# Kernel tuning notes

Measured on AMD Instinct MI355X. Metric: run time of the kernel, lower is better.

## Reference

```python
import jax, jax.numpy as jnp
import numpy as np

N = 100_000        # nodes
E = 1_600_000      # edges
IN_F = 128         # input_features
HID = 64           # hiddens per head
OUT = 64           # outputs
NHEADS = 8
ALPHA = 0.2        # leaky_relu negative slope


def setup_inputs() -> dict:
    key = jax.random.key(0)
    ks = jax.random.split(key, 8)
    x = jax.random.normal(ks[0], (N, IN_F), jnp.float32)
    edges = jax.random.randint(ks[1], (2, E), 0, N)
    # nn.Linear(input_features, input_features)
    W0 = jax.random.normal(ks[2], (IN_F, IN_F), jnp.float32) / np.sqrt(IN_F).astype(np.float32)
    b0 = jnp.zeros((IN_F,), jnp.float32)
    # per-head SpGAT params: W [in, out], a [2*out]
    W_heads = jax.random.normal(ks[3], (NHEADS, IN_F, HID), jnp.float32) * 0.05
    a_heads = jax.random.normal(ks[4], (NHEADS, 2 * HID), jnp.float32) * 0.05
    W_end = jax.random.normal(ks[5], (NHEADS * HID, OUT), jnp.float32) * 0.05
    a_end = jax.random.normal(ks[6], (2 * OUT,), jnp.float32) * 0.05
    return dict(x=x, edges=edges, W0=W0, b0=b0,
                W_heads=W_heads, a_heads=a_heads, W_end=W_end, a_end=a_end)


def _sp_gat_layer(x, src, dst, W, a, apply_elu):
    """Standard sparse GAT layer (pyGAT SpGraphAttentionLayer).

    score_e = a . [h_src || h_dst];  e = exp(-leaky_relu(score))
    out_i = (sum_{e: src=i} e * h_dst) / (sum_{e: src=i} e)
    """
    n = x.shape[0]
    h = x @ W                      # [N, F]
    F = h.shape[1]
    # a.[h_i||h_j] decomposed into per-node scores to avoid [E, 2F] gather
    s_src = h @ a[:F]              # [N]
    s_dst = h @ a[F:]              # [N]
    score = s_src[src] + s_dst[dst]            # [E]
    edge_e = jnp.exp(-jax.nn.leaky_relu(score, ALPHA))
    rowsum = jax.ops.segment_sum(edge_e, src, num_segments=n)            # [N]
    agg = jax.ops.segment_sum(edge_e[:, None] * h[dst], src, num_segments=n)  # [N, F]
    out = agg / (rowsum[:, None] + 1e-16)
    return jax.nn.elu(out) if apply_elu else out


def reference(x, edges, W0, b0, W_heads, a_heads, W_end, a_end):
    src, dst = edges[0], edges[1]
    xp = x @ W0 + b0                                           # self.layer
    # multi-head attention, concat on feature dim (loop over fixed small head count)
    heads = [_sp_gat_layer(xp, src, dst, W_heads[i], a_heads[i], apply_elu=True)
             for i in range(NHEADS)]
    h = jnp.concatenate(heads, axis=1)                         # [N, NHEADS*HID]
    out = _sp_gat_layer(h, src, dst, W_end, a_end, apply_elu=False)  # [N, OUT]
    return jax.nn.softmax(out, axis=1)
```

## Files before the change

kernel.cpp:

```cpp
#include <hip/hip_runtime.h>


using bf16x8 = __bf16 __attribute__((ext_vector_type(8)));
using f32x4  = float  __attribute__((ext_vector_type(4)));

__device__ __forceinline__ unsigned short f2bf(float f) {
    __bf16 h = (__bf16)f;
    return __builtin_bit_cast(unsigned short, h);
}
__device__ __forceinline__ float bflo(unsigned int u) {
    return __builtin_bit_cast(float, u << 16);
}
__device__ __forceinline__ float bfhi(unsigned int u) {
    return __builtin_bit_cast(float, u & 0xffff0000u);
}
__device__ __forceinline__ float bfs(unsigned short u) {
    return __builtin_bit_cast(float, (unsigned)u << 16);
}
__device__ __forceinline__ int rdlane_i(int v, int l) {
    return __builtin_amdgcn_readlane(v, l);
}
__device__ __forceinline__ float rdlane_f(float v, int l) {
    return __builtin_bit_cast(float, __builtin_amdgcn_readlane(__builtin_bit_cast(int, v), l));
}
__device__ __forceinline__ int rfl(int v) {
    return __builtin_amdgcn_readfirstlane(v);
}
__device__ __forceinline__ float exp2fast(float x) {
#if __has_builtin(__builtin_amdgcn_exp2f)
    return __builtin_amdgcn_exp2f(x);
#else
    return exp2f(x);
#endif
}

#define ALPHA_NEG 0.2f
#define LOG2E 1.44269504088896340736f
#define CHUNK 20000
#define TILE 4096
#define VPT 16

__global__ void pack_all(const float* __restrict__ W0, const float* __restrict__ Wh,
                         const float* __restrict__ We, const float* __restrict__ ah,
                         unsigned short* __restrict__ W0t, unsigned short* __restrict__ Ballt,
                         unsigned short* __restrict__ Wendt, unsigned short* __restrict__ Bscore) {
    int b = blockIdx.x, t = threadIdx.x;
    if (b < 64) {
        int idx = b * 256 + t;
        int n = idx >> 7, k = idx & 127;
        W0t[n * 128 + k] = f2bf(W0[k * 128 + n]);
    } else if (b < 320) {
        int idx = (b - 64) * 256 + t;
        int c = idx >> 7, k = idx & 127;
        int h = c >> 6, f = c & 63;
        Ballt[idx] = f2bf(Wh[(h * 128 + k) * 64 + f]);
    } else if (b < 448) {
        int idx = (b - 320) * 256 + t;
        int n = idx >> 9, k = idx & 511;
        Wendt[idx] = f2bf(We[k * 64 + n]);
    } else {
        int idx = (b - 448) * 256 + t;
        if (idx < 1024) {
            int h = idx >> 7, k = idx & 127;
            float s = 0.f, d = 0.f;
            for (int f = 0; f < 64; f++) {
                float wv = Wh[(h * 128 + k) * 64 + f];
                s += wv * ah[h * 128 + f];
                d += wv * ah[h * 128 + 64 + f];
            }
            Bscore[h * 128 + k] = f2bf(s * LOG2E);
            Bscore[(8 + h) * 128 + k] = f2bf(d * LOG2E);
        }
    }
}

__global__ void csr_hist(const int* __restrict__ src, int* __restrict__ hb, int E) {
    __shared__ int h[512];
    int t = threadIdx.x, blk = blockIdx.x;
    h[t] = 0; h[t + 256] = 0;
    __syncthreads();
    int base = blk * TILE + t;
#pragma unroll
    for (int v = 0; v < VPT; v++) {
        int e = base + v * 256;
        if (e < E) atomicAdd(&h[src[e] >> 8], 1);
    }
    __syncthreads();
    hb[blk * 512 + t] = h[t];
    hb[blk * 512 + t + 256] = h[t + 256];
}

__global__ void csr_scan(int* __restrict__ hb, int* __restrict__ bkt_base, int ablk) {
    __shared__ int s[512];
    int t = threadIdx.x;
    int run = 0;
    for (int b0 = 0; b0 < ablk; b0 += 8) {
        int vv[8];
#pragma unroll
        for (int u = 0; u < 8; u++) {
            int blk = b0 + u;
            vv[u] = (blk < ablk) ? hb[blk * 512 + t] : 0;
        }
#pragma unroll
        for (int u = 0; u < 8; u++) {
            int blk = b0 + u;
            if (blk < ablk) hb[blk * 512 + t] = run;
            run += vv[u];
        }
    }
    s[t] = run;
    __syncthreads();
    for (int off = 1; off < 512; off <<= 1) {
        int add = (t >= off) ? s[t - off] : 0;
        __syncthreads();
        s[t] += add;
        __syncthreads();
    }
    bkt_base[t] = s[t] - run;
}

__global__ void csr_scatter(const int* __restrict__ src, const int* __restrict__ dst,
                            const int* __restrict__ hb, const int* __restrict__ bkt_base,
                            int2* __restrict__ pairs, int E) {
    __shared__ int cur[512];
    int t = threadIdx.x, blk = blockIdx.x;
    cur[t]       = hb[blk * 512 + t]       + bkt_base[t];
    cur[t + 256] = hb[blk * 512 + t + 256] + bkt_base[t + 256];
    __syncthreads();
    int base = blk * TILE + t;
#pragma unroll
    for (int v = 0; v < VPT; v++) {
        int e = base + v * 256;
        if (e < E) {
            int sv = src[e], dv = dst[e];
            int pos = atomicAdd(&cur[sv >> 8], 1);
            pairs[pos] = make_int2(sv, dv);
        }
    }
}

__global__ void csr_build(const int2* __restrict__ pairs, const int* __restrict__ bkt_base,
                          int* __restrict__ row_ptr, int* __restrict__ dstp, int n) {
    __shared__ int h[256];
    __shared__ int sc[256];
    int t = threadIdx.x, b = blockIdx.x;
    int e0 = bkt_base[b], e1 = bkt_base[b + 1];
    h[t] = 0;
    __syncthreads();
    for (int e = e0 + t; e < e1; e += 256) atomicAdd(&h[pairs[e].x & 255], 1);
    __syncthreads();
    int v = h[t];
    sc[t] = v;
    __syncthreads();
    for (int off = 1; off < 256; off <<= 1) {
        int add = (t >= off) ? sc[t - off] : 0;
        __syncthreads();
        sc[t] += add;
        __syncthreads();
    }
    int excl = sc[t] - v;
    int gid = (b << 8) + t;
    if (gid <= n) row_ptr[gid] = e0 + excl;
    h[t] = excl;
    __syncthreads();
    for (int e = e0 + t; e < e1; e += 256) {
        int2 pr = pairs[e];
        int pos = atomicAdd(&h[pr.x & 255], 1);
        dstp[e0 + pos] = pr.y;
    }
}

template <int BM, int BN, int K, int WM, int WN, int MT, int NT,
          bool AF32, bool BIAS, bool OBF16, bool ELU, bool BATCHZ>
__launch_bounds__(256)
__global__ void gemm_mfma(const void* __restrict__ Ap, const unsigned short* __restrict__ Bt,
                          const float* __restrict__ bias, void* __restrict__ Cp, int M,
                          int lda, int ldc) {
    constexpr int LDK = 40;
    __shared__ unsigned short As[BM * LDK];
    __shared__ unsigned short Bs[BN * LDK];
    const int t = threadIdx.x;
    const long m0 = (long)blockIdx.x * BM;
    const long n0 = (long)blockIdx.y * BN;
    const int abase = BATCHZ ? blockIdx.z * K : 0;
    const unsigned short* Btz = BATCHZ ? Bt + (size_t)blockIdx.z * BN * K : Bt;
    const long cbase = BATCHZ ? (long)blockIdx.z * BN : 0;
    const int wave = t >> 6, lane = t & 63;
    const int wm = wave / WN, wn = wave % WN;
    const int lrow = lane & 15, lq = lane >> 4;

    f32x4 acc[MT][NT];
#pragma unroll
    for (int a = 0; a < MT; a++)
#pragma unroll
        for (int b = 0; b < NT; b++) acc[a][b] = (f32x4)0.0f;

    for (int kt = 0; kt < K / 32; kt++) {
        const int k0 = kt * 32;
        if constexpr (AF32) {
            const float* A = (const float*)Ap;
#pragma unroll
            for (int it = 0; it < BM * 8 / 256; it++) {
                int L = t + 256 * it;
                int row = L >> 3, kc = (L & 7) * 4;
                long gr = m0 + row;
                float4 v = make_float4(0.f, 0.f, 0.f, 0.f);
                if (gr < M) v = *(const float4*)&A[gr * lda + abase + k0 + kc];
                unsigned int lo = (unsigned)f2bf(v.x) | ((unsigned)f2bf(v.y) << 16);
                unsigned int hi = (unsigned)f2bf(v.z) | ((unsigned)f2bf(v.w) << 16);
                *(uint2*)&As[row * LDK + kc] = make_uint2(lo, hi);
            }
        } else {
            const unsigned short* A = (const unsigned short*)Ap;
#pragma unroll
            for (int it = 0; it < BM * 4 / 256; it++) {
                int L = t + 256 * it;
                int row = L >> 2, kc = (L & 3) * 8;
                long gr = m0 + row;
                uint4 v = make_uint4(0u, 0u, 0u, 0u);
                if (gr < M) v = *(const uint4*)&A[gr * lda + abase + k0 + kc];
                *(uint4*)&As[row * LDK + kc] = v;
            }
        }
#pragma unroll
        for (int it = 0; it < (BN * 4 + 255) / 256; it++) {
            int L = t + 256 * it;
            if (L < BN * 4) {
                int row = L >> 2, kc = (L & 3) * 8;
                *(uint4*)&Bs[row * LDK + kc] = *(const uint4*)&Btz[(n0 + row) * K + k0 + kc];
            }
        }
        __syncthreads();

        bf16x8 af[MT], bfr[NT];
#pragma unroll
        for (int mt = 0; mt < MT; mt++)
            af[mt] = *(const bf16x8*)&As[((wm * MT + mt) * 16 + lrow) * LDK + lq * 8];
#pragma unroll
        for (int nt = 0; nt < NT; nt++)
            bfr[nt] = *(const bf16x8*)&Bs[((wn * NT + nt) * 16 + lrow) * LDK + lq * 8];
#pragma unroll
        for (int mt = 0; mt < MT; mt++)
#pragma unroll
            for (int nt = 0; nt < NT; nt++)
                acc[mt][nt] = __builtin_amdgcn_mfma_f32_16x16x32_bf16(af[mt], bfr[nt],
                                                                     acc[mt][nt], 0, 0, 0);
        __syncthreads();
    }

#pragma unroll
    for (int mt = 0; mt < MT; mt++) {
        long rbase = m0 + (wm * MT + mt) * 16 + lq * 4;
#pragma unroll
        for (int nt = 0; nt < NT; nt++) {
            long col = cbase + n0 + (wn * NT + nt) * 16 + lrow;
            float bv = 0.f;
            if constexpr (BIAS) bv = bias[col];
#pragma unroll
            for (int r = 0; r < 4; r++) {
                long row = rbase + r;
                if (row < M) {
                    float v = acc[mt][nt][r] + bv;
                    if constexpr (ELU) v = v > 0.f ? v : __expf(v) - 1.0f;
                    if constexpr (OBF16)
                        ((unsigned short*)Cp)[row * ldc + col] = f2bf(v);
                    else
                        ((float*)Cp)[row * ldc + col] = v;
                }
            }
        }
    }
}

__global__ void agg_xp(const int* __restrict__ row_ptr, const int* __restrict__ dstp,
                       const float* __restrict__ s16,
                       const unsigned short* __restrict__ xp, unsigned short* __restrict__ z,
                       int n0, int n1) {
    int t = threadIdx.x, wave = t >> 6, lane = t & 63;
    int i = n0 + blockIdx.x * 4 + wave;
    if (i >= n1) return;
    int e0 = rfl(row_ptr[i]);
    int e1 = rfl(row_ptr[i + 1]);
    const int hl = lane & 7, sub8 = lane >> 3;
    const int voff = lane << 1;
    float ssv = s16[(size_t)i * 16 + hl];
    float acc[16];
#pragma unroll
    for (int c = 0; c < 16; c++) acc[c] = 0.f;
    float rsl = 0.f;

    for (int base = e0; base < e1; base += 64) {
        int m = e1 - base; if (m > 64) m = 64;
        int jl = lane < m ? lane : m - 1;
        int jreg = dstp[base + jl];

        for (int p = 0; p < m; p += 8) {
            int rel = p + sub8;
            bool ok = rel < m;
            if (!ok) rel = m - 1;
            int jw = __shfl(jreg, rel, 64);
            float sc = s16[(size_t)(unsigned)jw * 16 + 8 + hl];
            float s = ssv + sc;
            s = fmaxf(s, ALPHA_NEG * s);
            float wv = ok ? exp2fast(-s) : 0.f;
            rsl += wv;
            int nem = m - p;
            unsigned xv[8];
#pragma unroll
            for (int u = 0; u < 8; u++) {
                if (u < nem) {
                    int ju = rdlane_i(jreg, p + u);
                    xv[u] = *(const unsigned*)&xp[(size_t)(unsigned)ju * 128 + voff];
                }
            }
#pragma unroll
            for (int u = 0; u < 8; u++) {
                if (u < nem) {
                    float lo = bflo(xv[u]), hi = bfhi(xv[u]);
#pragma unroll
                    for (int h = 0; h < 8; h++) {
                        float wh = rdlane_f(wv, u * 8 + h);
                        acc[2 * h]     += wh * lo;
                        acc[2 * h + 1] += wh * hi;
                    }
                }
            }
        }
    }

    rsl += __shfl_xor(rsl, 8, 64);
    rsl += __shfl_xor(rsl, 16, 64);
    rsl += __shfl_xor(rsl, 32, 64);
    float inv = 1.0f / (rsl + 1e-16f);
    size_t zb = (size_t)(i - n0) * 1024 + voff;
#pragma unroll
    for (int h = 0; h < 8; h++) {
        float ih = rdlane_f(inv, h);
        unsigned pw = (unsigned)f2bf(acc[2 * h] * ih) |
                      ((unsigned)f2bf(acc[2 * h + 1] * ih) << 16);
        *(unsigned*)&z[zb + h * 128] = pw;
    }
}

__global__ void scores2(const unsigned short* __restrict__ h2b, const float* __restrict__ ae,
                        float* __restrict__ ss2, float* __restrict__ sd2, int n) {
    int t = threadIdx.x, wave = t >> 6, lane = t & 63;
    int i = blockIdx.x * 4 + wave;
    if (i >= n) return;
    float v = bfs(h2b[(size_t)i * 64 + lane]);
    float a = v * ae[lane];
    float b = v * ae[64 + lane];
    for (int d = 32; d > 0; d >>= 1) {
        a += __shfl_xor(a, d, 64);
        b += __shfl_xor(b, d, 64);
    }
    if (lane == 0) { ss2[i] = a * LOG2E; sd2[i] = b * LOG2E; }
}

__global__ void agg_final(const int* __restrict__ row_ptr, const int* __restrict__ dstp,
                          const float* __restrict__ ss2, const float* __restrict__ sd2,
                          const unsigned short* __restrict__ h2b, float* __restrict__ out,
                          int n) {
    int t = threadIdx.x, wave = t >> 6, lane = t & 63;
    int i = blockIdx.x * 4 + wave;
    if (i >= n) return;
    int e0 = rfl(row_ptr[i]);
    int e1 = rfl(row_ptr[i + 1]);
    float ssrc = ss2[i];
    float acc = 0.f, rsl = 0.f;
    for (int base = e0; base < e1; base += 64) {
        int cnt = e1 - base; if (cnt > 64) cnt = 64;
        int jv = 0; float wv = 0.f;
        if (lane < cnt) {
            jv = dstp[base + lane];
            float sc = ssrc + sd2[jv];
            sc = fmaxf(sc, ALPHA_NEG * sc);
            wv = exp2fast(-sc);
        }
        rsl += wv;
        int q = 0;
        for (; q + 8 <= cnt; q += 8) {
            float vv[8], ww[8];
#pragma unroll
            for (int u = 0; u < 8; u++) {
                int j = rdlane_i(jv, q + u);
                vv[u] = bfs(h2b[((size_t)(unsigned)j << 6) + lane]);
                ww[u] = rdlane_f(wv, q + u);
            }
#pragma unroll
            for (int u = 0; u < 8; u++) acc += ww[u] * vv[u];
        }
        for (; q < cnt; q++) {
            int j = rdlane_i(jv, q);
            float w = rdlane_f(wv, q);
            acc += w * bfs(h2b[((size_t)(unsigned)j << 6) + lane]);
        }
    }
    float rs = rsl;
    for (int d = 32; d > 0; d >>= 1) rs += __shfl_xor(rs, d, 64);
    float o = acc / (rs + 1e-16f);
    float m = o;
    for (int d = 32; d > 0; d >>= 1) m = fmaxf(m, __shfl_xor(m, d, 64));
    float e = __expf(o - m);
    float s = e;
    for (int d = 32; d > 0; d >>= 1) s += __shfl_xor(s, d, 64);
    out[(size_t)i * 64 + lane] = e / s;
}

extern "C" void kernel_launch(void* const* d_in, const int* in_sizes, int n_in,
                              void* d_out, int out_size, void* d_ws, size_t ws_size,
                              hipStream_t stream) {
    const float* x  = (const float*)d_in[0];
    const int* edges = (const int*)d_in[1];
    const float* W0 = (const float*)d_in[2];
    const float* b0 = (const float*)d_in[3];
    const float* Wh = (const float*)d_in[4];
    const float* ah = (const float*)d_in[5];
    const float* We = (const float*)d_in[6];
    const float* ae = (const float*)d_in[7];
    float* dout = (float*)d_out;

    const int Nn = in_sizes[0] / 128;
    const int E  = in_sizes[1] / 2;
    const int* src = edges;
    const int* dst = edges + E;

    char* p = (char*)d_ws;
    auto alloc = [&](size_t bytes) -> char* {
        char* r = p;
        p += (bytes + 255) & ~(size_t)255;
        return r;
    };
    unsigned short* W0t   = (unsigned short*)alloc(128 * 128 * 2);
    unsigned short* Ballt = (unsigned short*)alloc(512 * 128 * 2);
    unsigned short* Wendt = (unsigned short*)alloc((size_t)64 * 512 * 2);
    unsigned short* Bscore = (unsigned short*)alloc(16 * 128 * 2);
    const int ablk = (E + TILE - 1) / TILE;
    int* hist_blk = (int*)alloc((size_t)ablk * 512 * 4);
    int* bkt_base = (int*)alloc(512 * 4);
    int* row_ptr = (int*)alloc((size_t)(Nn + 1) * 4);
    int* dstp    = (int*)alloc((size_t)E * 4);
    float* s16   = (float*)alloc((size_t)Nn * 16 * 4);
    float* ss2   = (float*)alloc((size_t)Nn * 4);
    float* sd2   = (float*)alloc((size_t)Nn * 4);
    unsigned short* xp = (unsigned short*)alloc((size_t)Nn * 128 * 2);
    unsigned short* z  = (unsigned short*)alloc((size_t)CHUNK * 1024 * 2);
    unsigned short* hcat = (unsigned short*)alloc((size_t)Nn * 512 * 2);
    unsigned short* h2b = (unsigned short*)z;
    int2* pairs = (int2*)hcat;

    size_t needed = (size_t)(p - (char*)d_ws);
    if (needed > ws_size) return;

    const int gm = (Nn + 127) / 128;
    const int nbkt = (Nn + 255) >> 8;

    pack_all<<<452, 256, 0, stream>>>(W0, Wh, We, ah, W0t, Ballt, Wendt, Bscore);

    csr_hist<<<ablk, 256, 0, stream>>>(src, hist_blk, E);
    csr_scan<<<1, 512, 0, stream>>>(hist_blk, bkt_base, ablk);
    csr_scatter<<<ablk, 256, 0, stream>>>(src, dst, hist_blk, bkt_base, pairs, E);
    csr_build<<<nbkt, 256, 0, stream>>>(pairs, bkt_base, row_ptr, dstp, Nn);

    gemm_mfma<128, 128, 128, 2, 2, 4, 4, true, true, true, false, false>
        <<<dim3(gm, 1), 256, 0, stream>>>(x, W0t, b0, xp, Nn, 128, 128);

    gemm_mfma<128, 16, 128, 4, 1, 2, 1, false, false, false, false, false>
        <<<dim3(gm, 1), 256, 0, stream>>>(xp, Bscore, nullptr, s16, Nn, 128, 16);

    for (int c0 = 0; c0 < Nn; c0 += CHUNK) {
        int c1 = min(c0 + CHUNK, Nn);
        int Mc = c1 - c0;
        agg_xp<<<(Mc + 3) / 4, 256, 0, stream>>>(row_ptr, dstp, s16, xp, z, c0, c1);
        gemm_mfma<128, 64, 128, 4, 1, 2, 4, false, false, true, true, true>
            <<<dim3((Mc + 127) / 128, 1, 8), 256, 0, stream>>>(
                z, Ballt, nullptr, hcat + (size_t)c0 * 512, Mc, 1024, 512);
    }

    gemm_mfma<128, 64, 512, 4, 1, 2, 4, false, false, true, false, false>
        <<<dim3(gm, 1), 256, 0, stream>>>(hcat, Wendt, nullptr, h2b, Nn, 512, 64);

    scores2<<<(Nn + 3) / 4, 256, 0, stream>>>(h2b, ae, ss2, sd2, Nn);
    agg_final<<<(Nn + 3) / 4, 256, 0, stream>>>(row_ptr, dstp, ss2, sd2, h2b, dout, Nn);
}
```

Baseline: 561.4 us.

## Fuse neighbor aggregation with per-head projection GEMM via shared-memory staging

Replaces the chunked agg_xp plus batched per-head GEMM launches with a single agg_gemm kernel. Each block aggregates 16 nodes into an LDS tile and immediately runs MFMA against the per-head weights, applying ELU and writing hcat directly. This removes the global round trip of the large intermediate z buffer and about ten kernel launches. In exchange, each block uses about 33 KB of LDS, which may lower occupancy for the latency-bound gather, and the B fragments are read directly from global memory.

```diff
diff --git a/kernel.cpp b/kernel.cpp
--- a/kernel.cpp
+++ b/kernel.cpp
@@ -36,9 +36,10 @@
 
 #define ALPHA_NEG 0.2f
 #define LOG2E 1.44269504088896340736f
-#define CHUNK 20000
 #define TILE 4096
 #define VPT 16
+#define NB 16
+#define LDKZ 1032
 
 __global__ void pack_all(const float* __restrict__ W0, const float* __restrict__ Wh,
                          const float* __restrict__ We, const float* __restrict__ ah,
@@ -171,7 +172,7 @@
 }
 
 template <int BM, int BN, int K, int WM, int WN, int MT, int NT,
-          bool AF32, bool BIAS, bool OBF16, bool ELU, bool BATCHZ>
+          bool AF32, bool BIAS, bool OBF16, bool ELU>
 __launch_bounds__(256)
 __global__ void gemm_mfma(const void* __restrict__ Ap, const unsigned short* __restrict__ Bt,
                           const float* __restrict__ bias, void* __restrict__ Cp, int M,
@@ -181,10 +182,6 @@
     __shared__ unsigned short Bs[BN * LDK];
     const int t = threadIdx.x;
     const long m0 = (long)blockIdx.x * BM;
-    const long n0 = (long)blockIdx.y * BN;
-    const int abase = BATCHZ ? blockIdx.z * K : 0;
-    const unsigned short* Btz = BATCHZ ? Bt + (size_t)blockIdx.z * BN * K : Bt;
-    const long cbase = BATCHZ ? (long)blockIdx.z * BN : 0;
     const int wave = t >> 6, lane = t & 63;
     const int wm = wave / WN, wn = wave % WN;
     const int lrow = lane & 15, lq = lane >> 4;
@@ -205,7 +202,7 @@
                 int row = L >> 3, kc = (L & 7) * 4;
                 long gr = m0 + row;
                 float4 v = make_float4(0.f, 0.f, 0.f, 0.f);
-                if (gr < M) v = *(const float4*)&A[gr * lda + abase + k0 + kc];
+                if (gr < M) v = *(const float4*)&A[gr * lda + k0 + kc];
                 unsigned int lo = (unsigned)f2bf(v.x) | ((unsigned)f2bf(v.y) << 16);
                 unsigned int hi = (unsigned)f2bf(v.z) | ((unsigned)f2bf(v.w) << 16);
                 *(uint2*)&As[row * LDK + kc] = make_uint2(lo, hi);
@@ -218,7 +215,7 @@
                 int row = L >> 2, kc = (L & 3) * 8;
                 long gr = m0 + row;
                 uint4 v = make_uint4(0u, 0u, 0u, 0u);
-                if (gr < M) v = *(const uint4*)&A[gr * lda + abase + k0 + kc];
+                if (gr < M) v = *(const uint4*)&A[gr * lda + k0 + kc];
                 *(uint4*)&As[row * LDK + kc] = v;
             }
         }
@@ -227,7 +224,7 @@
             int L = t + 256 * it;
             if (L < BN * 4) {
                 int row = L >> 2, kc = (L & 3) * 8;
-                *(uint4*)&Bs[row * LDK + kc] = *(const uint4*)&Btz[(n0 + row) * K + k0 + kc];
+                *(uint4*)&Bs[row * LDK + kc] = *(const uint4*)&Bt[(size_t)row * K + k0 + kc];
             }
         }
         __syncthreads();
@@ -253,7 +250,7 @@
         long rbase = m0 + (wm * MT + mt) * 16 + lq * 4;
 #pragma unroll
         for (int nt = 0; nt < NT; nt++) {
-            long col = cbase + n0 + (wn * NT + nt) * 16 + lrow;
+            long col = (wn * NT + nt) * 16 + lrow;
             float bv = 0.f;
             if constexpr (BIAS) bv = bias[col];
 #pragma unroll
@@ -272,73 +269,119 @@
     }
 }
 
-__global__ void agg_xp(const int* __restrict__ row_ptr, const int* __restrict__ dstp,
-                       const float* __restrict__ s16,
-                       const unsigned short* __restrict__ xp, unsigned short* __restrict__ z,
-                       int n0, int n1) {
+__launch_bounds__(256)
+__global__ void agg_gemm(const int* __restrict__ row_ptr, const int* __restrict__ dstp,
+                         const float* __restrict__ s16, const unsigned short* __restrict__ xp,
+                         const unsigned short* __restrict__ Ballt,
+                         unsigned short* __restrict__ hcat, int n) {
+    __shared__ unsigned short zs[NB * LDKZ];
     int t = threadIdx.x, wave = t >> 6, lane = t & 63;
-    int i = n0 + blockIdx.x * 4 + wave;
-    if (i >= n1) return;
-    int e0 = rfl(row_ptr[i]);
-    int e1 = rfl(row_ptr[i + 1]);
     const int hl = lane & 7, sub8 = lane >> 3;
     const int voff = lane << 1;
-    float ssv = s16[(size_t)i * 16 + hl];
-    float acc[16];
-#pragma unroll
-    for (int c = 0; c < 16; c++) acc[c] = 0.f;
-    float rsl = 0.f;
-
-    for (int base = e0; base < e1; base += 64) {
-        int m = e1 - base; if (m > 64) m = 64;
-        int jl = lane < m ? lane : m - 1;
-        int jreg = dstp[base + jl];
-
-        for (int p = 0; p < m; p += 8) {
-            int rel = p + sub8;
-            bool ok = rel < m;
-            if (!ok) rel = m - 1;
-            int jw = __shfl(jreg, rel, 64);
-            float sc = s16[(size_t)(unsigned)jw * 16 + 8 + hl];
-            float s = ssv + sc;
-            s = fmaxf(s, ALPHA_NEG * s);
-            float wv = ok ? exp2fast(-s) : 0.f;
-            rsl += wv;
-            int nem = m - p;
-            unsigned xv[8];
-#pragma unroll
-            for (int u = 0; u < 8; u++) {
-                if (u < nem) {
-                    int ju = rdlane_i(jreg, p + u);
-                    xv[u] = *(const unsigned*)&xp[(size_t)(unsigned)ju * 128 + voff];
-                }
-            }
-#pragma unroll
-            for (int u = 0; u < 8; u++) {
-                if (u < nem) {
-                    float lo = bflo(xv[u]), hi = bfhi(xv[u]);
-#pragma unroll
-                    for (int h = 0; h < 8; h++) {
-                        float wh = rdlane_f(wv, u * 8 + h);
-                        acc[2 * h]     += wh * lo;
-                        acc[2 * h + 1] += wh * hi;
+    const int nbase = blockIdx.x * NB;
+
+    for (int nn = 0; nn < NB / 4; nn++) {
+        int ln = wave * (NB / 4) + nn;
+        int i = nbase + ln;
+        float acc[16];
+#pragma unroll
+        for (int c = 0; c < 16; c++) acc[c] = 0.f;
+        float rsl = 0.f;
+        if (i < n) {
+            int e0 = rfl(row_ptr[i]);
+            int e1 = rfl(row_ptr[i + 1]);
+            float ssv = s16[(size_t)i * 16 + hl];
+            for (int base = e0; base < e1; base += 64) {
+                int mm = e1 - base; if (mm > 64) mm = 64;
+                int jl = lane < mm ? lane : mm - 1;
+                int jreg = dstp[base + jl];
+                for (int p = 0; p < mm; p += 8) {
+                    int rel = p + sub8;
+                    bool ok = rel < mm;
+                    if (!ok) rel = mm - 1;
+                    int jw = __shfl(jreg, rel, 64);
+                    float sc = s16[(size_t)(unsigned)jw * 16 + 8 + hl];
+                    float s = ssv + sc;
+                    s = fmaxf(s, ALPHA_NEG * s);
+                    float wv = ok ? exp2fast(-s) : 0.f;
+                    rsl += wv;
+                    int nem = mm - p;
+                    unsigned xv[8];
+#pragma unroll
+                    for (int u = 0; u < 8; u++) {
+                        if (u < nem) {
+                            int ju = rdlane_i(jreg, p + u);
+                            xv[u] = *(const unsigned*)&xp[(size_t)(unsigned)ju * 128 + voff];
+                        }
+                    }
+#pragma unroll
+                    for (int u = 0; u < 8; u++) {
+                        if (u < nem) {
+                            float lo = bflo(xv[u]), hi = bfhi(xv[u]);
+#pragma unroll
+                            for (int h = 0; h < 8; h++) {
+                                float wh = rdlane_f(wv, u * 8 + h);
+                                acc[2 * h]     += wh * lo;
+                                acc[2 * h + 1] += wh * hi;
+                            }
+                        }
                     }
                 }
             }
         }
-    }
-
-    rsl += __shfl_xor(rsl, 8, 64);
-    rsl += __shfl_xor(rsl, 16, 64);
-    rsl += __shfl_xor(rsl, 32, 64);
-    float inv = 1.0f / (rsl + 1e-16f);
-    size_t zb = (size_t)(i - n0) * 1024 + voff;
-#pragma unroll
-    for (int h = 0; h < 8; h++) {
-        float ih = rdlane_f(inv, h);
-        unsigned pw = (unsigned)f2bf(acc[2 * h] * ih) |
-                      ((unsigned)f2bf(acc[2 * h + 1] * ih) << 16);
-        *(unsigned*)&z[zb + h * 128] = pw;
+        rsl += __shfl_xor(rsl, 8, 64);
+        rsl += __shfl_xor(rsl, 16, 64);
+        rsl += __shfl_xor(rsl, 32, 64);
+        float inv = 1.0f / (rsl + 1e-16f);
+#pragma unroll
+        for (int h = 0; h < 8; h++) {
+            float ih = rdlane_f(inv, h);
+            unsigned pw = (unsigned)f2bf(acc[2 * h] * ih) |
+                          ((unsigned)f2bf(acc[2 * h + 1] * ih) << 16);
+            *(unsigned*)&zs[ln * LDKZ + h * 128 + voff] = pw;
+        }
+    }
+    __syncthreads();
+
+    const int lrow = lane & 15, lq = lane >> 4;
+    f32x4 acc2[2][4];
+#pragma unroll
+    for (int a = 0; a < 2; a++)
+#pragma unroll
+        for (int b = 0; b < 4; b++) acc2[a][b] = (f32x4)0.0f;
+
+#pragma unroll
+    for (int hh = 0; hh < 2; hh++) {
+        int h = wave * 2 + hh;
+#pragma unroll
+        for (int kt = 0; kt < 4; kt++) {
+            bf16x8 af = *(const bf16x8*)&zs[lrow * LDKZ + h * 128 + kt * 32 + lq * 8];
+#pragma unroll
+            for (int nt = 0; nt < 4; nt++) {
+                bf16x8 bfr = *(const bf16x8*)&Ballt[(size_t)(h * 64 + nt * 16 + lrow) * 128
+                                                    + kt * 32 + lq * 8];
+                acc2[hh][nt] = __builtin_amdgcn_mfma_f32_16x16x32_bf16(af, bfr,
+                                                                      acc2[hh][nt], 0, 0, 0);
+            }
+        }
+    }
+
+#pragma unroll
+    for (int hh = 0; hh < 2; hh++) {
+        int h = wave * 2 + hh;
+#pragma unroll
+        for (int nt = 0; nt < 4; nt++) {
+            int col = h * 64 + nt * 16 + lrow;
+#pragma unroll
+            for (int r = 0; r < 4; r++) {
+                int row = nbase + lq * 4 + r;
+                if (row < n) {
+                    float v = acc2[hh][nt][r];
+                    v = v > 0.f ? v : __expf(v) - 1.0f;
+                    hcat[(size_t)row * 512 + col] = f2bf(v);
+                }
+            }
+        }
     }
 }
 
@@ -444,9 +487,8 @@
     float* ss2   = (float*)alloc((size_t)Nn * 4);
     float* sd2   = (float*)alloc((size_t)Nn * 4);
     unsigned short* xp = (unsigned short*)alloc((size_t)Nn * 128 * 2);
-    unsigned short* z  = (unsigned short*)alloc((size_t)CHUNK * 1024 * 2);
     unsigned short* hcat = (unsigned short*)alloc((size_t)Nn * 512 * 2);
-    unsigned short* h2b = (unsigned short*)z;
+    unsigned short* h2b = (unsigned short*)alloc((size_t)Nn * 64 * 2);
     int2* pairs = (int2*)hcat;
 
     size_t needed = (size_t)(p - (char*)d_ws);
@@ -462,22 +504,16 @@
     csr_scatter<<<ablk, 256, 0, stream>>>(src, dst, hist_blk, bkt_base, pairs, E);
     csr_build<<<nbkt, 256, 0, stream>>>(pairs, bkt_base, row_ptr, dstp, Nn);
 
-    gemm_mfma<128, 128, 128, 2, 2, 4, 4, true, true, true, false, false>
+    gemm_mfma<128, 128, 128, 2, 2, 4, 4, true, true, true, false>
         <<<dim3(gm, 1), 256, 0, stream>>>(x, W0t, b0, xp, Nn, 128, 128);
 
-    gemm_mfma<128, 16, 128, 4, 1, 2, 1, false, false, false, false, false>
+    gemm_mfma<128, 16, 128, 4, 1, 2, 1, false, false, false, false>
         <<<dim3(gm, 1), 256, 0, stream>>>(xp, Bscore, nullptr, s16, Nn, 128, 16);
 
-    for (int c0 = 0; c0 < Nn; c0 += CHUNK) {
-        int c1 = min(c0 + CHUNK, Nn);
-        int Mc = c1 - c0;
-        agg_xp<<<(Mc + 3) / 4, 256, 0, stream>>>(row_ptr, dstp, s16, xp, z, c0, c1);
-        gemm_mfma<128, 64, 128, 4, 1, 2, 4, false, false, true, true, true>
-            <<<dim3((Mc + 127) / 128, 1, 8), 256, 0, stream>>>(
-                z, Ballt, nullptr, hcat + (size_t)c0 * 512, Mc, 1024, 512);
-    }
-
-    gemm_mfma<128, 64, 512, 4, 1, 2, 4, false, false, true, false, false>
+    agg_gemm<<<(Nn + NB - 1) / NB, 256, 0, stream>>>(row_ptr, dstp, s16, xp,
+                                                     Ballt, hcat, Nn);
+
+    gemm_mfma<128, 64, 512, 4, 1, 2, 4, false, false, true, false>
         <<<dim3(gm, 1), 256, 0, stream>>>(hcat, Wendt, nullptr, h2b, Nn, 512, 64);
 
     scores2<<<(Nn + 3) / 4, 256, 0, stream>>>(h2b, ae, ss2, sd2, Nn);
```

Result: faster. 526.0 us (-6.3%).
